# Kernel optimization log

Hardware: AMD Instinct MI355X
Metric: run time of the kernel (lower is better)

The kernel has to match this reference:

```python
import jax, jax.numpy as jnp
import numpy as np
import math

B, T, D = 8, 512, 512
H_HEADS, DQ, DV = 8, 64, 64
N_LAYERS, D_HID = 6, 2048
VOCAB, N_CLASSES = 32000, 5
LN_EPS = 1e-5


def setup_inputs() -> dict:
    key = jax.random.key(0)
    ks = jax.random.split(key, 20)
    s = 0.02
    x = jax.random.randint(ks[0], (B, T), 0, VOCAB - 1)
    emb = jax.random.normal(ks[1], (VOCAB, D), jnp.float32) * s
    emb = emb.at[VOCAB - 1].set(0.0)  # padding_idx row is zero
    # per-layer params stacked on leading N axis; weights stored [in, out]
    Wq = jax.random.normal(ks[2], (N_LAYERS, D, H_HEADS * DQ), jnp.float32) * s
    bq = jnp.zeros((N_LAYERS, H_HEADS * DQ), jnp.float32)
    Wk = jax.random.normal(ks[3], (N_LAYERS, D, H_HEADS * DQ), jnp.float32) * s
    bk = jnp.zeros((N_LAYERS, H_HEADS * DQ), jnp.float32)
    Wv = jax.random.normal(ks[4], (N_LAYERS, D, H_HEADS * DV), jnp.float32) * s
    bv = jnp.zeros((N_LAYERS, H_HEADS * DV), jnp.float32)
    Wo = jax.random.normal(ks[5], (N_LAYERS, H_HEADS * DV, D), jnp.float32) * s
    bo = jnp.zeros((N_LAYERS, D), jnp.float32)
    gamma = jnp.ones((N_LAYERS, D), jnp.float32)
    beta = jnp.zeros((N_LAYERS, D), jnp.float32)
    W1 = jax.random.normal(ks[6], (N_LAYERS, D, D_HID), jnp.float32) * s
    b1 = jnp.zeros((N_LAYERS, D_HID), jnp.float32)
    W2 = jax.random.normal(ks[7], (N_LAYERS, D_HID, D), jnp.float32) * s
    b2 = jnp.zeros((N_LAYERS, D), jnp.float32)
    Wout = jax.random.normal(ks[8], (D * T, N_CLASSES), jnp.float32) * s
    bout = jnp.zeros((N_CLASSES,), jnp.float32)
    return dict(x=x, stage=0, emb=emb, Wq=Wq, bq=bq, Wk=Wk, bk=bk, Wv=Wv, bv=bv,
                Wo=Wo, bo=bo, gamma=gamma, beta=beta, W1=W1, b1=b1, W2=W2, b2=b2,
                Wout=Wout, bout=bout)


def _sinusoidal_pe(t, d):
    pos = jnp.arange(t, dtype=jnp.float32)[:, None]              # [T,1]
    inv = jnp.exp(jnp.arange(0, d, 2, dtype=jnp.float32) * (-math.log(10000.0) / d))
    ang = pos * inv[None, :]                                     # [T, D/2]
    pe = jnp.ones((t, d), jnp.float32)
    pe = pe.at[:, 0::2].set(jnp.sin(ang)).at[:, 1::2].set(jnp.cos(ang))
    return pe


def _layer_norm(x, g, b):
    mu = jnp.mean(x, -1, keepdims=True)
    var = jnp.mean((x - mu) ** 2, -1, keepdims=True)
    return g * (x - mu) * jax.lax.rsqrt(var + LN_EPS) + b


def _attn(x, wq, bq_, wk, bk_, wv, bv_, wo, bo_):
    b, t, _ = x.shape
    q = (x @ wq + bq_).reshape(b, t, H_HEADS, DQ).transpose(0, 2, 1, 3)  # [B,h,T,dq]
    k = (x @ wk + bk_).reshape(b, t, H_HEADS, DQ).transpose(0, 2, 1, 3)
    v = (x @ wv + bv_).reshape(b, t, H_HEADS, DV).transpose(0, 2, 1, 3)
    score = jnp.einsum('bhtd,bhsd->bhts', q, k)  # NOTE: no 1/sqrt(d) scaling, per source
    a = jax.nn.softmax(score, axis=-1)
    o = jnp.einsum('bhts,bhsv->bhtv', a, v)
    o = o.transpose(0, 2, 1, 3).reshape(b, t, H_HEADS * DV)
    return o @ wo + bo_


def reference(x, stage, emb, Wq, bq, Wk, bk, Wv, bv, Wo, bo, gamma, beta, W1, b1, W2, b2, Wout, bout):
    h = emb[x]                                   # [B,T,D]
    h = h + _sinusoidal_pe(h.shape[1], h.shape[2])[None]
    for i in range(N_LAYERS):
        res = h
        a = _attn(h, Wq[i], bq[i], Wk[i], bk[i], Wv[i], bv[i], Wo[i], bo[i])
        h = _layer_norm(a + res, gamma[i], beta[i])
        res = h
        f = jax.nn.relu(h @ W1[i] + b1[i]) @ W2[i] + b2[i]
        h = _layer_norm(f + res, gamma[i], beta[i])  # same LN params reused, per source
    out = h.reshape(h.shape[0], -1) @ Wout + bout
    return out
```

## Files before the change

### kernel.cpp

```cpp
#include <hip/hip_runtime.h>
#include <hip/hip_bf16.h>


typedef _Float16 f16_t;
typedef _Float16 f16x8 __attribute__((ext_vector_type(8)));
typedef _Float16 f16x4 __attribute__((ext_vector_type(4)));
typedef _Float16 f16x2 __attribute__((ext_vector_type(2)));
typedef float    f32x4 __attribute__((ext_vector_type(4)));

#define LSTR 3145728LL

__device__ __forceinline__ void gl_lds16(const f16_t* g, f16_t* l) {
    __builtin_amdgcn_global_load_lds(
        (const __attribute__((address_space(1))) unsigned int*)g,
        (__attribute__((address_space(3))) unsigned int*)l, 16, 0, 0);
}

template<int BM, int BN, int WR, int WC, int OUTF16, int RELU>
__global__ void __launch_bounds__(256)
gemm_kernel(const f16_t* __restrict__ A, const f16_t* __restrict__ B,
            const float* __restrict__ bias, void* __restrict__ Cout,
            int M, int N, int K, int lda, int ldb, int ldc, int zmod,
            long long sAhi, long long sAlo, long long sBhi, long long sBlo,
            long long sChi, long long sClo)
{
    constexpr int BK  = 32;
    constexpr int WMT = BM / WR;
    constexpr int WNT = BN / WC;
    constexpr int MR  = WMT / 16;
    constexpr int NR  = WNT / 16;
    constexpr int IA  = BM / 64;
    constexpr int IB  = BN / 64;
    __shared__ __align__(16) f16_t As[2][BM][BK];
    __shared__ __align__(16) f16_t Bs[2][BN][BK];

    const int tid  = threadIdx.x;
    const int wid  = tid >> 6, lane = tid & 63;
    const int wr   = wid / WC, wc = wid % WC;
    const int z    = blockIdx.z;
    const int zh   = z / zmod, zl = z % zmod;
    const f16_t* Ab = A + (long long)zh * sAhi + (long long)zl * sAlo;
    const f16_t* Bb = B + (long long)zh * sBhi + (long long)zl * sBlo;
    const int m0 = blockIdx.x * BM;
    const int n0 = blockIdx.y * BN;

    f32x4 acc[MR][NR] = {};

    const f16_t* srcA[IA]; const f16_t* srcB[IB];
#pragma unroll
    for (int i = 0; i < IA; ++i) {
        const int c = i * 256 + tid, row = c >> 2;
        const int kch = (c & 3) ^ ((row >> 1) & 3);
        srcA[i] = Ab + (long long)(m0 + row) * lda + kch * 8;
    }
#pragma unroll
    for (int i = 0; i < IB; ++i) {
        const int c = i * 256 + tid, row = c >> 2;
        const int kch = (c & 3) ^ ((row >> 1) & 3);
        srcB[i] = Bb + (long long)(n0 + row) * ldb + kch * 8;
    }
    auto stage = [&](int bf_, int t) {
        const int k0 = t * BK;
#pragma unroll
        for (int i = 0; i < IA; ++i)
            gl_lds16(srcA[i] + k0, &As[bf_][0][0] + (i * 256 + wid * 64) * 8);
#pragma unroll
        for (int i = 0; i < IB; ++i)
            gl_lds16(srcB[i] + k0, &Bs[bf_][0][0] + (i * 256 + wid * 64) * 8);
    };

    const int l15 = lane & 15;
    const int kc  = (lane >> 4) * 8;
    int aoff[MR], boff[NR];
#pragma unroll
    for (int m = 0; m < MR; ++m) {
        const int row = wr * WMT + m * 16 + l15;
        aoff[m] = ((row * BK + kc) * 2) ^ (((row >> 1) & 3) << 4);
    }
#pragma unroll
    for (int n = 0; n < NR; ++n) {
        const int row = wc * WNT + n * 16 + l15;
        boff[n] = ((row * BK + kc) * 2) ^ (((row >> 1) & 3) << 4);
    }

    const int NT = K / BK;
    stage(0, 0);
    __syncthreads();

    int buf = 0;
    for (int t = 0; t < NT; ++t) {
        if (t + 1 < NT) stage(buf ^ 1, t + 1);
        const char* Al = (const char*)&As[buf][0][0];
        const char* Bl = (const char*)&Bs[buf][0][0];
        f16x8 af[MR], bfr[NR];
#pragma unroll
        for (int m = 0; m < MR; ++m) af[m]  = *(const f16x8*)(Al + aoff[m]);
#pragma unroll
        for (int n = 0; n < NR; ++n) bfr[n] = *(const f16x8*)(Bl + boff[n]);
#pragma unroll
        for (int m = 0; m < MR; ++m)
#pragma unroll
            for (int n = 0; n < NR; ++n)
                acc[m][n] = __builtin_amdgcn_mfma_f32_16x16x32_f16(af[m], bfr[n], acc[m][n], 0, 0, 0);
        __syncthreads();
        buf ^= 1;
    }

    const long long cOff = (long long)zh * sChi + (long long)zl * sClo;
    const int rbase = (lane >> 4) * 4;
#pragma unroll
    for (int m = 0; m < MR; ++m) {
        const int row = m0 + wr * WMT + m * 16 + rbase;
#pragma unroll
        for (int n = 0; n < NR; ++n) {
            const int col = n0 + wc * WNT + n * 16 + l15;
            const float bb = bias ? bias[col] : 0.0f;
#pragma unroll
            for (int r = 0; r < 4; ++r) {
                float v = acc[m][n][r] + bb;
                if (RELU) v = fmaxf(v, 0.0f);
                const long long idx = cOff + (long long)(row + r) * ldc + col;
                if (OUTF16) ((f16_t*)Cout)[idx] = (f16_t)v;
                else        ((float*)Cout)[idx] = v;
            }
        }
    }
}

__global__ void __launch_bounds__(256)
attn_flash_kernel(const f16_t* __restrict__ qkv, const f16_t* __restrict__ Vt,
                  f16_t* __restrict__ ao)
{
    __shared__ __align__(16) f16_t Ks[512 * 64];
    __shared__ __align__(16) f16_t Qs[64 * 64];
    __shared__ __align__(16) f16_t Ps[4][16 * 64];
    const int tid = threadIdx.x, wid = tid >> 6, lane = tid & 63;
    const int l15 = lane & 15, g = lane >> 4;
    const int z = blockIdx.y, b = z >> 3, hh = z & 7;
    const int q0 = blockIdx.x * 64;
    const f16_t* Kbase = qkv + (long long)b * 512 * 1536 + 512 + hh * 64;
    const f16_t* Qbase = qkv + (long long)(b * 512 + q0) * 1536 + hh * 64;
    const f16_t* Vbase = Vt + (long long)z * 32768;

#pragma unroll
    for (int i = 0; i < 16; ++i) {
        const int c = i * 256 + tid, t = c >> 3, j = c & 7;
        gl_lds16(Kbase + (long long)t * 1536 + ((j ^ (t & 7)) << 3), Ks + c * 8);
    }
#pragma unroll
    for (int i = 0; i < 2; ++i) {
        const int c = i * 256 + tid, t = c >> 3, j = c & 7;
        gl_lds16(Qbase + (long long)t * 1536 + ((j ^ (t & 7)) << 3), Qs + c * 8);
    }
    __syncthreads();

    const int q = wid * 16 + l15;
    f16x8 qf[2];
#pragma unroll
    for (int k = 0; k < 2; ++k)
        qf[k] = *(const f16x8*)(Qs + q * 64 + (((k * 4 + g) ^ (l15 & 7)) << 3));

    f32x4 ov[4] = {};
    float m_run = -1e30f, l_run = 0.0f;
    f16_t* Pw = &Ps[wid][0];

    for (int ck = 0; ck < 8; ++ck) {
        const int kc0 = ck * 64;
        f16x8 vf[4][2];
#pragma unroll
        for (int n = 0; n < 4; ++n)
#pragma unroll
            for (int k = 0; k < 2; ++k)
                vf[n][k] = *(const f16x8*)(Vbase + (n * 16 + l15) * 512 + kc0 + k * 32 + g * 8);
        f32x4 s[4] = {};
#pragma unroll
        for (int k = 0; k < 2; ++k)
#pragma unroll
            for (int m = 0; m < 4; ++m) {
                const int key = kc0 + m * 16 + l15;
                const f16x8 a = *(const f16x8*)(Ks + key * 64 + (((k * 4 + g) ^ (key & 7)) << 3));
                s[m] = __builtin_amdgcn_mfma_f32_16x16x32_f16(a, qf[k], s[m], 0, 0, 0);
            }
        float cmax = -1e30f;
#pragma unroll
        for (int m = 0; m < 4; ++m)
#pragma unroll
            for (int r = 0; r < 4; ++r) cmax = fmaxf(cmax, s[m][r]);
        cmax = fmaxf(cmax, __shfl_xor(cmax, 16, 64));
        cmax = fmaxf(cmax, __shfl_xor(cmax, 32, 64));
        const float mnew = fmaxf(m_run, cmax);
        const float corr = __expf(m_run - mnew);
        float csum = 0.0f;
#pragma unroll
        for (int m = 0; m < 4; ++m) {
            f16x4 p4;
#pragma unroll
            for (int r = 0; r < 4; ++r) {
                const float pe = __expf(s[m][r] - mnew);
                csum += pe;
                p4[r] = (f16_t)pe;
            }
            *(f16x4*)(Pw + l15 * 64 + ((((m * 2 + (g >> 1)) ^ (l15 & 7))) << 3) + ((g & 1) << 2)) = p4;
        }
        csum += __shfl_xor(csum, 16, 64);
        csum += __shfl_xor(csum, 32, 64);
        l_run = l_run * corr + csum;
        m_run = mnew;
        float cr[4];
#pragma unroll
        for (int r = 0; r < 4; ++r) cr[r] = __shfl(corr, g * 4 + r, 64);
#pragma unroll
        for (int n = 0; n < 4; ++n)
#pragma unroll
            for (int r = 0; r < 4; ++r) ov[n][r] *= cr[r];
#pragma unroll
        for (int k = 0; k < 2; ++k) {
            const f16x8 pf = *(const f16x8*)(Pw + l15 * 64 + (((k * 4 + g) ^ (l15 & 7)) << 3));
#pragma unroll
            for (int n = 0; n < 4; ++n)
                ov[n] = __builtin_amdgcn_mfma_f32_16x16x32_f16(pf, vf[n][k], ov[n], 0, 0, 0);
        }
    }

    const float inv = 1.0f / l_run;
    float ir[4];
#pragma unroll
    for (int r = 0; r < 4; ++r) ir[r] = __shfl(inv, g * 4 + r, 64);
#pragma unroll
    for (int n = 0; n < 4; ++n)
#pragma unroll
        for (int r = 0; r < 4; ++r) {
            const long long row = b * 512 + q0 + wid * 16 + g * 4 + r;
            ao[row * 512 + hh * 64 + n * 16 + l15] = (f16_t)(ov[n][r] * ir[r]);
        }
}

__global__ void wconv_kernel(const float* __restrict__ Wq, const float* __restrict__ Wk,
                             const float* __restrict__ Wv, const float* __restrict__ Wo,
                             const float* __restrict__ W1, const float* __restrict__ W2,
                             f16_t* __restrict__ wT)
{
    __shared__ float tile[32][33];
    const int t     = blockIdx.x;
    const int layer = t / 3072;
    const int r     = t % 3072;
    const float* src; f16_t* dst; int R, C, tt;
    if (r < 1024) {
        const int mat = r >> 8; tt = r & 255; R = 512; C = 512;
        const float* s4 = (mat == 0) ? Wq : (mat == 1) ? Wk : (mat == 2) ? Wv : Wo;
        src = s4 + (long long)layer * 262144;
        dst = wT + (long long)layer * LSTR + (long long)mat * 262144;
    } else if (r < 2048) {
        tt = r - 1024; R = 512; C = 2048;
        src = W1 + (long long)layer * 1048576;
        dst = wT + (long long)layer * LSTR + 1048576;
    } else {
        tt = r - 2048; R = 2048; C = 512;
        src = W2 + (long long)layer * 1048576;
        dst = wT + (long long)layer * LSTR + 2097152;
    }
    const int tC = C >> 5;
    const int tr = tt / tC, tc = tt % tC;
    const int r0 = tr * 32, c0 = tc * 32;
    const int tx = threadIdx.x, ty = threadIdx.y;
#pragma unroll
    for (int i = 0; i < 4; ++i)
        tile[ty + 8 * i][tx] = src[(long long)(r0 + ty + 8 * i) * C + c0 + tx];
    __syncthreads();
#pragma unroll
    for (int i = 0; i < 4; ++i)
        dst[(long long)(c0 + ty + 8 * i) * R + r0 + tx] = (f16_t)tile[tx][ty + 8 * i];
}

__global__ void biascat_kernel(const float* __restrict__ bq, const float* __restrict__ bk,
                               const float* __restrict__ bv, float* __restrict__ qkvb)
{
    const int i = blockIdx.x * 256 + threadIdx.x;
    if (i >= 9216) return;
    const int l = i / 1536, c = i % 1536;
    float v;
    if (c < 512)       v = bq[l * 512 + c];
    else if (c < 1024) v = bk[l * 512 + c - 512];
    else               v = bv[l * 512 + c - 1024];
    qkvb[i] = v;
}

__global__ void embed_kernel(const int* __restrict__ xt, const float* __restrict__ emb,
                             f16_t* __restrict__ hb)
{
    const int row = blockIdx.x;
    const int t   = row & 511;
    const int tok = xt[row];
    const int tid = threadIdx.x;
#pragma unroll
    for (int s = 0; s < 2; ++s) {
        const int d = tid + s * 256;
        const int i = d >> 1;
        const float inv = expf((float)(2 * i) * (-9.210340371976184f / 512.0f));
        const float ang = (float)t * inv;
        const float pe  = (d & 1) ? cosf(ang) : sinf(ang);
        hb[(long long)row * 512 + d] = (f16_t)(emb[(long long)tok * 512 + d] + pe);
    }
}

__global__ void add_ln_kernel(const f16_t* __restrict__ X, int ns, long long sstr,
                              const float* __restrict__ bias,
                              const float* __restrict__ g, const float* __restrict__ b,
                              f16_t* __restrict__ Hf)
{
    __shared__ float red[4], red2[4];
    const long long row = blockIdx.x;
    f16_t* h = Hf + row * 512;
    const int tid = threadIdx.x;
    const int c0 = 2 * tid;
    const f16x2 hv = *(const f16x2*)&h[c0];
    float s0 = (float)hv[0] + bias[c0];
    float s1 = (float)hv[1] + bias[c0 + 1];
    for (int s = 0; s < ns; ++s) {
        const f16x2 xv = *(const f16x2*)&X[s * sstr + row * 512 + c0];
        s0 += (float)xv[0];
        s1 += (float)xv[1];
    }
    float sum = s0 + s1, sq = s0 * s0 + s1 * s1;
#pragma unroll
    for (int o = 32; o > 0; o >>= 1) { sum += __shfl_down(sum, o, 64); sq += __shfl_down(sq, o, 64); }
    if ((tid & 63) == 0) { red[tid >> 6] = sum; red2[tid >> 6] = sq; }
    __syncthreads();
    sum = red[0] + red[1] + red[2] + red[3];
    sq  = red2[0] + red2[1] + red2[2] + red2[3];
    const float mu = sum * (1.0f / 512.0f);
    float var = sq * (1.0f / 512.0f) - mu * mu;
    var = fmaxf(var, 0.0f);
    const float rs = rsqrtf(var + 1e-5f);
    f16x2 o2;
    o2[0] = (f16_t)(g[c0]     * (s0 - mu) * rs + b[c0]);
    o2[1] = (f16_t)(g[c0 + 1] * (s1 - mu) * rs + b[c0 + 1]);
    *(f16x2*)&h[c0] = o2;
}

__global__ void vtrans_kernel(const f16_t* __restrict__ qkv, f16_t* __restrict__ Vt)
{
    __shared__ f16_t tl[32][34];
    const int z  = blockIdx.y;
    const int b  = z >> 3, hh = z & 7;
    const int tile = blockIdx.x;
    const int tr = tile >> 1, tc = tile & 1;
    const int t0 = tr * 32, c0 = tc * 32;
    const int tx = threadIdx.x, ty = threadIdx.y;
#pragma unroll
    for (int i = 0; i < 4; ++i)
        tl[ty + 8 * i][tx] = qkv[(long long)(b * 512 + t0 + ty + 8 * i) * 1536 + 1024 + hh * 64 + c0 + tx];
    __syncthreads();
#pragma unroll
    for (int i = 0; i < 4; ++i)
        Vt[((long long)z * 64 + c0 + ty + 8 * i) * 512 + t0 + tx] = tl[tx][ty + 8 * i];
}

__global__ void head_partial_kernel(const f16_t* __restrict__ hb, const float* __restrict__ Wout,
                                    float* __restrict__ partials)
{
    const int blk = blockIdx.x;
    const int b = blk >> 6, chunk = blk & 63;
    const int tid = threadIdx.x;
    const f16_t* hp = hb + (long long)b * 262144 + (long long)chunk * 4096;
    float a0 = 0, a1 = 0, a2 = 0, a3 = 0, a4 = 0;
    for (int it = 0; it < 16; ++it) {
        const int idx = it * 256 + tid;
        const float hv = (float)hp[idx];
        const float* w = Wout + ((long long)chunk * 4096 + idx) * 5;
        a0 += hv * w[0]; a1 += hv * w[1]; a2 += hv * w[2]; a3 += hv * w[3]; a4 += hv * w[4];
    }
#pragma unroll
    for (int o = 32; o > 0; o >>= 1) {
        a0 += __shfl_down(a0, o, 64); a1 += __shfl_down(a1, o, 64); a2 += __shfl_down(a2, o, 64);
        a3 += __shfl_down(a3, o, 64); a4 += __shfl_down(a4, o, 64);
    }
    __shared__ float sm[4][5];
    const int lane = tid & 63, w = tid >> 6;
    if (lane == 0) { sm[w][0] = a0; sm[w][1] = a1; sm[w][2] = a2; sm[w][3] = a3; sm[w][4] = a4; }
    __syncthreads();
    if (tid < 5)
        partials[(long long)blk * 5 + tid] = sm[0][tid] + sm[1][tid] + sm[2][tid] + sm[3][tid];
}

__global__ void head_final_kernel(const float* __restrict__ partials, const float* __restrict__ bout,
                                  float* __restrict__ out)
{
    const int tid = threadIdx.x;
    if (tid >= 40) return;
    const int b = tid / 5, c = tid % 5;
    float s = bout[c];
    const float* p = partials + (long long)b * 64 * 5 + c;
    for (int ck = 0; ck < 64; ++ck) s += p[ck * 5];
    out[tid] = s;
}

extern "C" void kernel_launch(void* const* d_in, const int* in_sizes, int n_in,
                              void* d_out, int out_size, void* d_ws, size_t ws_size,
                              hipStream_t stream)
{
    (void)in_sizes; (void)n_in; (void)out_size; (void)ws_size;
    const int*   x_tok = (const int*)  d_in[0];
    const float* emb   = (const float*)d_in[2];
    const float* Wq    = (const float*)d_in[3];
    const float* bq    = (const float*)d_in[4];
    const float* Wk    = (const float*)d_in[5];
    const float* bk    = (const float*)d_in[6];
    const float* Wv    = (const float*)d_in[7];
    const float* bv    = (const float*)d_in[8];
    const float* Wo    = (const float*)d_in[9];
    const float* bo    = (const float*)d_in[10];
    const float* gma   = (const float*)d_in[11];
    const float* bta   = (const float*)d_in[12];
    const float* W1    = (const float*)d_in[13];
    const float* b1    = (const float*)d_in[14];
    const float* W2    = (const float*)d_in[15];
    const float* b2    = (const float*)d_in[16];
    const float* Wout  = (const float*)d_in[17];
    const float* bout  = (const float*)d_in[18];

    char* ws = (char*)d_ws;
    size_t off = 0;
    auto take = [&](size_t bytes) { char* p = ws + off; off += (bytes + 255) & ~(size_t)255; return p; };
    f16_t* wT    = (f16_t*)take(18874368ULL * 2);
    f16_t* hb    = (f16_t*)take(2097152ULL * 2);
    f16_t* qkv   = (f16_t*)take(6291456ULL * 2);
    f16_t* Vt    = (f16_t*)take(2097152ULL * 2);
    f16_t* ao    = (f16_t*)take(2097152ULL * 2);
    f16_t* f1    = (f16_t*)take(8388608ULL * 2);
    f16_t* t16   = (f16_t*)take(4ULL * 2097152ULL * 2);
    float* qkvb  = (float*)take(9216ULL * 4);
    float* parts = (float*)take(2560ULL * 4);

    wconv_kernel <<<dim3(18432), dim3(32, 8), 0, stream>>>(Wq, Wk, Wv, Wo, W1, W2, wT);
    biascat_kernel<<<dim3(36), 256, 0, stream>>>(bq, bk, bv, qkvb);
    embed_kernel <<<dim3(4096), 256, 0, stream>>>(x_tok, emb, hb);

    for (int l = 0; l < 6; ++l) {
        const f16_t* wl = wT + (long long)l * LSTR;
        gemm_kernel<64,128,2,2,1,0><<<dim3(64,12,1),256,0,stream>>>(hb, wl, qkvb + l*1536, qkv,
            4096,1536,512, 512,512,1536, 1, 0,0,0,0,0,0);
        vtrans_kernel<<<dim3(32,64), dim3(32,8), 0, stream>>>(qkv, Vt);
        attn_flash_kernel<<<dim3(8,64),256,0,stream>>>(qkv, Vt, ao);
        gemm_kernel<64,128,2,2,1,0><<<dim3(64,4,2),256,0,stream>>>(ao, wl + 786432, nullptr, t16,
            4096,512,256, 512,512,512, 1, 256LL,0LL, 256LL,0LL, 2097152LL,0LL);
        add_ln_kernel<<<dim3(4096),256,0,stream>>>(t16, 2, 2097152LL, bo + l*512,
            gma + l*512, bta + l*512, hb);
        gemm_kernel<128,128,2,2,1,1><<<dim3(32,16,1),256,0,stream>>>(hb, wl + 1048576, b1 + l*2048, f1,
            4096,2048,512, 512,512,2048, 1, 0,0,0,0,0,0);
        gemm_kernel<128,128,2,2,1,0><<<dim3(32,4,4),256,0,stream>>>(f1, wl + 2097152, nullptr, t16,
            4096,512,512, 2048,2048,512, 1, 512LL,0LL, 512LL,0LL, 2097152LL,0LL);
        add_ln_kernel<<<dim3(4096),256,0,stream>>>(t16, 4, 2097152LL, b2 + l*512,
            gma + l*512, bta + l*512, hb);
    }

    head_partial_kernel<<<dim3(512),256,0,stream>>>(hb, Wout, parts);
    head_final_kernel  <<<dim3(1),64,0,stream>>>(parts, bout, (float*)d_out);
}
```

Measured before the change: 624.5 us.

## Fuse V transpose into QKV GEMM, use BK=64 tiles, warp-per-row LayerNorm

```diff
diff --git a/kernel.cpp b/kernel.cpp
--- a/kernel.cpp
+++ b/kernel.cpp
@@ -16,21 +16,24 @@
         (__attribute__((address_space(3))) unsigned int*)l, 16, 0, 0);
 }
 
-template<int BM, int BN, int WR, int WC, int OUTF16, int RELU>
+template<int BM, int BN, int BK, int WR, int WC, int OUTF16, int RELU, int VOUT>
 __global__ void __launch_bounds__(256)
 gemm_kernel(const f16_t* __restrict__ A, const f16_t* __restrict__ B,
             const float* __restrict__ bias, void* __restrict__ Cout,
+            f16_t* __restrict__ vt,
             int M, int N, int K, int lda, int ldb, int ldc, int zmod,
             long long sAhi, long long sAlo, long long sBhi, long long sBlo,
             long long sChi, long long sClo)
 {
-    constexpr int BK  = 32;
     constexpr int WMT = BM / WR;
     constexpr int WNT = BN / WC;
     constexpr int MR  = WMT / 16;
     constexpr int NR  = WNT / 16;
-    constexpr int IA  = BM / 64;
-    constexpr int IB  = BN / 64;
+    constexpr int KK  = BK / 32;
+    constexpr int CPR = BK / 8;
+    constexpr int RS  = (BK == 32) ? 1 : 0;
+    constexpr int IA  = BM * BK / 2048;
+    constexpr int IB  = BN * BK / 2048;
     __shared__ __align__(16) f16_t As[2][BM][BK];
     __shared__ __align__(16) f16_t Bs[2][BN][BK];
 
@@ -49,14 +52,14 @@
     const f16_t* srcA[IA]; const f16_t* srcB[IB];
 #pragma unroll
     for (int i = 0; i < IA; ++i) {
-        const int c = i * 256 + tid, row = c >> 2;
-        const int kch = (c & 3) ^ ((row >> 1) & 3);
+        const int c = i * 256 + tid, row = c / CPR;
+        const int kch = (c % CPR) ^ ((row >> RS) & (CPR - 1));
         srcA[i] = Ab + (long long)(m0 + row) * lda + kch * 8;
     }
 #pragma unroll
     for (int i = 0; i < IB; ++i) {
-        const int c = i * 256 + tid, row = c >> 2;
-        const int kch = (c & 3) ^ ((row >> 1) & 3);
+        const int c = i * 256 + tid, row = c / CPR;
+        const int kch = (c % CPR) ^ ((row >> RS) & (CPR - 1));
         srcB[i] = Bb + (long long)(n0 + row) * ldb + kch * 8;
     }
     auto stage = [&](int bf_, int t) {
@@ -70,17 +73,23 @@
     };
 
     const int l15 = lane & 15;
-    const int kc  = (lane >> 4) * 8;
-    int aoff[MR], boff[NR];
+    const int g   = lane >> 4;
+    int aoff[MR][KK], boff[NR][KK];
 #pragma unroll
     for (int m = 0; m < MR; ++m) {
         const int row = wr * WMT + m * 16 + l15;
-        aoff[m] = ((row * BK + kc) * 2) ^ (((row >> 1) & 3) << 4);
+        const int swz = ((row >> RS) & (CPR - 1)) << 4;
+#pragma unroll
+        for (int kk = 0; kk < KK; ++kk)
+            aoff[m][kk] = ((row * BK + kk * 32 + g * 8) * 2) ^ swz;
     }
 #pragma unroll
     for (int n = 0; n < NR; ++n) {
         const int row = wc * WNT + n * 16 + l15;
-        boff[n] = ((row * BK + kc) * 2) ^ (((row >> 1) & 3) << 4);
+        const int swz = ((row >> RS) & (CPR - 1)) << 4;
+#pragma unroll
+        for (int kk = 0; kk < KK; ++kk)
+            boff[n][kk] = ((row * BK + kk * 32 + g * 8) * 2) ^ swz;
     }
 
     const int NT = K / BK;
@@ -92,16 +101,22 @@
         if (t + 1 < NT) stage(buf ^ 1, t + 1);
         const char* Al = (const char*)&As[buf][0][0];
         const char* Bl = (const char*)&Bs[buf][0][0];
-        f16x8 af[MR], bfr[NR];
-#pragma unroll
-        for (int m = 0; m < MR; ++m) af[m]  = *(const f16x8*)(Al + aoff[m]);
-#pragma unroll
-        for (int n = 0; n < NR; ++n) bfr[n] = *(const f16x8*)(Bl + boff[n]);
+        f16x8 af[MR][KK], bfr[NR][KK];
 #pragma unroll
         for (int m = 0; m < MR; ++m)
 #pragma unroll
-            for (int n = 0; n < NR; ++n)
-                acc[m][n] = __builtin_amdgcn_mfma_f32_16x16x32_f16(af[m], bfr[n], acc[m][n], 0, 0, 0);
+            for (int kk = 0; kk < KK; ++kk) af[m][kk] = *(const f16x8*)(Al + aoff[m][kk]);
+#pragma unroll
+        for (int n = 0; n < NR; ++n)
+#pragma unroll
+            for (int kk = 0; kk < KK; ++kk) bfr[n][kk] = *(const f16x8*)(Bl + boff[n][kk]);
+#pragma unroll
+        for (int kk = 0; kk < KK; ++kk)
+#pragma unroll
+            for (int m = 0; m < MR; ++m)
+#pragma unroll
+                for (int n = 0; n < NR; ++n)
+                    acc[m][n] = __builtin_amdgcn_mfma_f32_16x16x32_f16(af[m][kk], bfr[n][kk], acc[m][n], 0, 0, 0);
         __syncthreads();
         buf ^= 1;
     }
@@ -115,13 +130,22 @@
         for (int n = 0; n < NR; ++n) {
             const int col = n0 + wc * WNT + n * 16 + l15;
             const float bb = bias ? bias[col] : 0.0f;
-#pragma unroll
-            for (int r = 0; r < 4; ++r) {
-                float v = acc[m][n][r] + bb;
-                if (RELU) v = fmaxf(v, 0.0f);
-                const long long idx = cOff + (long long)(row + r) * ldc + col;
-                if (OUTF16) ((f16_t*)Cout)[idx] = (f16_t)v;
-                else        ((float*)Cout)[idx] = v;
+            if (VOUT && col >= 1024) {
+                const int hh = (col - 1024) >> 6, dv = (col - 1024) & 63;
+                const int bb_ = row >> 9, t0 = row & 511;
+                f16x4 v4;
+#pragma unroll
+                for (int r = 0; r < 4; ++r) v4[r] = (f16_t)(acc[m][n][r] + bb);
+                *(f16x4*)&vt[((long long)((bb_ * 8 + hh) * 64 + dv)) * 512 + t0] = v4;
+            } else {
+#pragma unroll
+                for (int r = 0; r < 4; ++r) {
+                    float v = acc[m][n][r] + bb;
+                    if (RELU) v = fmaxf(v, 0.0f);
+                    const long long idx = cOff + (long long)(row + r) * ldc + col;
+                    if (OUTF16) ((f16_t*)Cout)[idx] = (f16_t)v;
+                    else        ((float*)Cout)[idx] = v;
+                }
             }
         }
     }
@@ -303,57 +327,42 @@
     }
 }
 
-__global__ void add_ln_kernel(const f16_t* __restrict__ X, int ns, long long sstr,
-                              const float* __restrict__ bias,
-                              const float* __restrict__ g, const float* __restrict__ b,
-                              f16_t* __restrict__ Hf)
-{
-    __shared__ float red[4], red2[4];
-    const long long row = blockIdx.x;
+__global__ void __launch_bounds__(256)
+add_ln_kernel(const f16_t* __restrict__ X, int ns, long long sstr,
+              const float* __restrict__ bias,
+              const float* __restrict__ g, const float* __restrict__ b,
+              f16_t* __restrict__ Hf)
+{
+    const int wid = threadIdx.x >> 6, lane = threadIdx.x & 63;
+    const long long row = (long long)blockIdx.x * 4 + wid;
     f16_t* h = Hf + row * 512;
-    const int tid = threadIdx.x;
-    const int c0 = 2 * tid;
-    const f16x2 hv = *(const f16x2*)&h[c0];
-    float s0 = (float)hv[0] + bias[c0];
-    float s1 = (float)hv[1] + bias[c0 + 1];
+    const int c0 = lane * 8;
+    const f16x8 hv = *(const f16x8*)&h[c0];
+    float v[8];
+#pragma unroll
+    for (int e = 0; e < 8; ++e) v[e] = (float)hv[e] + bias[c0 + e];
     for (int s = 0; s < ns; ++s) {
-        const f16x2 xv = *(const f16x2*)&X[s * sstr + row * 512 + c0];
-        s0 += (float)xv[0];
-        s1 += (float)xv[1];
-    }
-    float sum = s0 + s1, sq = s0 * s0 + s1 * s1;
-#pragma unroll
-    for (int o = 32; o > 0; o >>= 1) { sum += __shfl_down(sum, o, 64); sq += __shfl_down(sq, o, 64); }
-    if ((tid & 63) == 0) { red[tid >> 6] = sum; red2[tid >> 6] = sq; }
-    __syncthreads();
-    sum = red[0] + red[1] + red[2] + red[3];
-    sq  = red2[0] + red2[1] + red2[2] + red2[3];
+        const f16x8 xv = *(const f16x8*)&X[s * sstr + row * 512 + c0];
+#pragma unroll
+        for (int e = 0; e < 8; ++e) v[e] += (float)xv[e];
+    }
+    float sum = 0.0f, sq = 0.0f;
+#pragma unroll
+    for (int e = 0; e < 8; ++e) { sum += v[e]; sq += v[e] * v[e]; }
+#pragma unroll
+    for (int o = 1; o < 64; o <<= 1) {
+        sum += __shfl_xor(sum, o, 64);
+        sq  += __shfl_xor(sq,  o, 64);
+    }
     const float mu = sum * (1.0f / 512.0f);
     float var = sq * (1.0f / 512.0f) - mu * mu;
     var = fmaxf(var, 0.0f);
     const float rs = rsqrtf(var + 1e-5f);
-    f16x2 o2;
-    o2[0] = (f16_t)(g[c0]     * (s0 - mu) * rs + b[c0]);
-    o2[1] = (f16_t)(g[c0 + 1] * (s1 - mu) * rs + b[c0 + 1]);
-    *(f16x2*)&h[c0] = o2;
-}
-
-__global__ void vtrans_kernel(const f16_t* __restrict__ qkv, f16_t* __restrict__ Vt)
-{
-    __shared__ f16_t tl[32][34];
-    const int z  = blockIdx.y;
-    const int b  = z >> 3, hh = z & 7;
-    const int tile = blockIdx.x;
-    const int tr = tile >> 1, tc = tile & 1;
-    const int t0 = tr * 32, c0 = tc * 32;
-    const int tx = threadIdx.x, ty = threadIdx.y;
-#pragma unroll
-    for (int i = 0; i < 4; ++i)
-        tl[ty + 8 * i][tx] = qkv[(long long)(b * 512 + t0 + ty + 8 * i) * 1536 + 1024 + hh * 64 + c0 + tx];
-    __syncthreads();
-#pragma unroll
-    for (int i = 0; i < 4; ++i)
-        Vt[((long long)z * 64 + c0 + ty + 8 * i) * 512 + t0 + tx] = tl[tx][ty + 8 * i];
+    f16x8 o8;
+#pragma unroll
+    for (int e = 0; e < 8; ++e)
+        o8[e] = (f16_t)(g[c0 + e] * (v[e] - mu) * rs + b[c0 + e]);
+    *(f16x8*)&h[c0] = o8;
 }
 
 __global__ void head_partial_kernel(const f16_t* __restrict__ hb, const float* __restrict__ Wout,
@@ -438,19 +447,18 @@
 
     for (int l = 0; l < 6; ++l) {
         const f16_t* wl = wT + (long long)l * LSTR;
-        gemm_kernel<64,128,2,2,1,0><<<dim3(64,12,1),256,0,stream>>>(hb, wl, qkvb + l*1536, qkv,
-            4096,1536,512, 512,512,1536, 1, 0,0,0,0,0,0);
-        vtrans_kernel<<<dim3(32,64), dim3(32,8), 0, stream>>>(qkv, Vt);
+        gemm_kernel<64,128,64,2,2,1,0,1><<<dim3(64,12,1),256,0,stream>>>(hb, wl, qkvb + l*1536,
+            qkv, Vt, 4096,1536,512, 512,512,1536, 1, 0,0,0,0,0,0);
         attn_flash_kernel<<<dim3(8,64),256,0,stream>>>(qkv, Vt, ao);
-        gemm_kernel<64,128,2,2,1,0><<<dim3(64,4,2),256,0,stream>>>(ao, wl + 786432, nullptr, t16,
-            4096,512,256, 512,512,512, 1, 256LL,0LL, 256LL,0LL, 2097152LL,0LL);
-        add_ln_kernel<<<dim3(4096),256,0,stream>>>(t16, 2, 2097152LL, bo + l*512,
+        gemm_kernel<64,128,64,2,2,1,0,0><<<dim3(64,4,2),256,0,stream>>>(ao, wl + 786432, nullptr,
+            t16, nullptr, 4096,512,256, 512,512,512, 1, 256LL,0LL, 256LL,0LL, 2097152LL,0LL);
+        add_ln_kernel<<<dim3(1024),256,0,stream>>>(t16, 2, 2097152LL, bo + l*512,
             gma + l*512, bta + l*512, hb);
-        gemm_kernel<128,128,2,2,1,1><<<dim3(32,16,1),256,0,stream>>>(hb, wl + 1048576, b1 + l*2048, f1,
-            4096,2048,512, 512,512,2048, 1, 0,0,0,0,0,0);
-        gemm_kernel<128,128,2,2,1,0><<<dim3(32,4,4),256,0,stream>>>(f1, wl + 2097152, nullptr, t16,
-            4096,512,512, 2048,2048,512, 1, 512LL,0LL, 512LL,0LL, 2097152LL,0LL);
-        add_ln_kernel<<<dim3(4096),256,0,stream>>>(t16, 4, 2097152LL, b2 + l*512,
+        gemm_kernel<64,128,64,2,2,1,1,0><<<dim3(64,16,1),256,0,stream>>>(hb, wl + 1048576, b1 + l*2048,
+            f1, nullptr, 4096,2048,512, 512,512,2048, 1, 0,0,0,0,0,0);
+        gemm_kernel<64,128,64,2,2,1,0,0><<<dim3(64,4,4),256,0,stream>>>(f1, wl + 2097152, nullptr,
+            t16, nullptr, 4096,512,512, 2048,2048,512, 1, 512LL,0LL, 512LL,0LL, 2097152LL,0LL);
+        add_ln_kernel<<<dim3(1024),256,0,stream>>>(t16, 4, 2097152LL, b2 + l*512,
             gma + l*512, bta + l*512, hb);
     }
 
```

New measurement: 588.7 us. 1.06x faster.
